# Performance work log

Measured on AMD Instinct MI355X. Metric: run time of the kernel, lower is better.

## Reference

```python
import jax, jax.numpy as jnp
import numpy as np

T, B, K = 512, 512, 8
V, H, NL, NLAB = 5, 30, 4, 3


def setup_inputs() -> dict:
    key = jax.random.key(0)
    ks = jax.random.split(key, 12)
    s = 0.1
    return {
        "x": jax.random.randint(ks[0], (T, B, K), 0, V),
        "weight_of_x": jax.random.uniform(ks[1], (T, B, K), dtype=jnp.float32),
        "embed": jax.random.normal(ks[2], (V, H), dtype=jnp.float32) * s,
        "lstm_Wih": jax.random.normal(ks[3], (NL, 4 * H, H), dtype=jnp.float32) * s,
        "lstm_Whh": jax.random.normal(ks[4], (NL, 4 * H, H), dtype=jnp.float32) * s,
        "lstm_bih": jax.random.normal(ks[5], (NL, 4 * H), dtype=jnp.float32) * s,
        "lstm_bhh": jax.random.normal(ks[6], (NL, 4 * H), dtype=jnp.float32) * s,
        "attn_W1": jax.random.normal(ks[7], (H, 64), dtype=jnp.float32) * s,
        "attn_b1": jnp.zeros((64,), jnp.float32),
        "attn_W2": jax.random.normal(ks[8], (64, 1), dtype=jnp.float32) * s,
        "attn_b2": jnp.zeros((1,), jnp.float32),
        "fc_W": jax.random.normal(ks[9], (H, NLAB), dtype=jnp.float32) * s,
        "fc_b": jnp.zeros((NLAB,), jnp.float32),
    }


def _lstm_layer(xs, Wih, Whh, bih, bhh):
    # xs: (T, B, H_in); PyTorch gate order i, f, g, o
    b = bih + bhh
    Bsz = xs.shape[1]
    h0 = jnp.zeros((Bsz, Whh.shape[1]), xs.dtype)

    def step(carry, xt):
        h, c = carry
        gates = xt @ Wih.T + h @ Whh.T + b  # (B, 4H)
        i, f, g, o = jnp.split(gates, 4, axis=-1)
        i, f, o = jax.nn.sigmoid(i), jax.nn.sigmoid(f), jax.nn.sigmoid(o)
        g = jnp.tanh(g)
        c = f * c + i * g
        h = o * jnp.tanh(c)
        return (h, c), h

    _, hs = jax.lax.scan(step, (h0, h0), xs)
    return hs  # (T, B, H)


def reference(x, weight_of_x, embed, lstm_Wih, lstm_Whh, lstm_bih, lstm_bhh,
              attn_W1, attn_b1, attn_W2, attn_b2, fc_W, fc_b):
    # embedding + weighted mean pooling over K
    e = embed[x] * weight_of_x[..., None]          # (T, B, K, H)
    e = jax.nn.relu(e)
    seq = jnp.mean(e, axis=2)                      # (T, B, H)

    # 4-layer LSTM (loop over fixed num_layers)
    out = seq
    for l in range(lstm_Wih.shape[0]):
        out = _lstm_layer(out, lstm_Wih[l], lstm_Whh[l], lstm_bih[l], lstm_bhh[l])

    # attention pooling over time
    enc = jnp.transpose(out, (1, 0, 2))            # (B, T, H)
    energy = jax.nn.relu(enc @ attn_W1 + attn_b1) @ attn_W2 + attn_b2  # (B, T, 1)
    weights = jax.nn.softmax(energy[..., 0], axis=1)  # (B, T)
    pooled = jnp.sum(enc * weights[..., None], axis=1)  # (B, H)

    # dropout is identity in eval mode
    logit = jax.nn.softmax(pooled @ fc_W + fc_b, axis=1)  # (B, 3)
    return logit
```

## Files before the change

kernel.cpp:

```cpp
#include <hip/hip_runtime.h>

#define TT 512
#define BB 512
#define KK 8
#define HH 30
#define GG 120
#define NLAYER 4

__device__ __forceinline__ float rcp_f(float x) { return __builtin_amdgcn_rcpf(x); }
__device__ __forceinline__ float rdlane_f(float v, int l) {
    return __int_as_float(__builtin_amdgcn_readlane(__float_as_int(v), l));
}
__device__ __forceinline__ float2 pk_fma_v(float2 a, float2 b, float2 c) {
    float2 d;
    asm("v_pk_fma_f32 %0, %1, %2, %3" : "=v"(d) : "v"(a), "v"(b), "v"(c));
    return d;
}
__device__ __forceinline__ float2 pk_fma_s(float2 a, float2 bs, float2 c) {
    float2 d;
    asm("v_pk_fma_f32 %0, %1, %2, %3" : "=v"(d) : "v"(a), "s"(bs), "v"(c));
    return d;
}
__device__ __forceinline__ float2 pk_add(float2 a, float2 b) {
    float2 d;
    asm("v_pk_add_f32 %0, %1, %2" : "=v"(d) : "v"(a), "v"(b));
    return d;
}
__device__ __forceinline__ float swap32_hi(float x) {
    float a = x, b = x;
    asm("v_permlane32_swap_b32 %0, %1" : "+v"(a), "+v"(b));
    return b;
}

__global__ __launch_bounds__(256) __attribute__((amdgpu_waves_per_eu(2, 2)))
void rnn_fused(
    const int*   __restrict__ xin,  const float* __restrict__ wxin,
    const float* __restrict__ embed,
    const float* __restrict__ Wih,  const float* __restrict__ Whh,
    const float* __restrict__ bih,  const float* __restrict__ bhh,
    const float* __restrict__ W1,   const float* __restrict__ b1,
    const float* __restrict__ W2,   const float* __restrict__ b2,
    const float* __restrict__ fcW,  const float* __restrict__ fcb,
    float* __restrict__ out)
{
    __shared__ alignas(16) float hstore[TT * HH];
    __shared__ alignas(16) float seqring[2][16][32];
    __shared__ alignas(16) int   ringx[4][16][KK];
    __shared__ alignas(16) float ringw[4][16][KK];
    __shared__ alignas(16) float hring[NLAYER][8][32];
    __shared__ alignas(16) float re_s[5 * HH];
    __shared__ alignas(16) float energy_s[TT];
    __shared__ float red_s[16];
    __shared__ float part_s[8][HH];
    __shared__ float pooled_s[HH];
    __shared__ float logits_s[3];
    __shared__ int   sync_s[8];

    const int tid  = threadIdx.x;
    const int wv   = tid >> 6;
    const int lane = tid & 63;
    const int b    = blockIdx.x;
    volatile int* vs = sync_s;

    if (tid < 8) sync_s[tid] = 0;
    if (tid < 5 * HH) re_s[tid] = fmaxf(embed[tid], 0.0f);
    {
        float4 z; z.x = 0.f; z.y = 0.f; z.z = 0.f; z.w = 0.f;
        ((float4*)hring)[tid] = z;
    }

    int4 hx = {0,0,0,0}; float4 hw = {0,0,0,0};
    if (wv == 0 && lane < 32) {
        const int r = lane >> 1, hf = lane & 1;
        #pragma unroll
        for (int cc = 0; cc < 2; ++cc) {
            long off = ((long)(16 * cc + r) * BB + b) * KK + hf * 4;
            *(int4*)(&ringx[cc][r][hf * 4])   = *(const int4*)(xin  + off);
            *(float4*)(&ringw[cc][r][hf * 4]) = *(const float4*)(wxin + off);
        }
        long off2 = ((long)(32 + r) * BB + b) * KK + hf * 4;
        hx = *(const int4*)(xin  + off2);
        hw = *(const float4*)(wxin + off2);
    }

    const int half = lane >> 5;
    const int q31  = lane & 31;
    const int qq   = (q31 < HH) ? q31 : (HH - 1);
    const int rA   = qq + half * HH;
    const int rB   = rA + 60;
    float2 wihA[15], wihB[15], whhA[15], whhB[15];
    {
        const float* WihL = Wih + wv * GG * HH;
        const float* WhhL = Whh + wv * GG * HH;
        #pragma unroll
        for (int kk = 0; kk < 15; ++kk) {
            wihA[kk] = *(const float2*)(WihL + rA * HH + 2 * kk);
            wihB[kk] = *(const float2*)(WihL + rB * HH + 2 * kk);
            whhA[kk] = *(const float2*)(WhhL + rA * HH + 2 * kk);
            whhB[kk] = *(const float2*)(WhhL + rB * HH + 2 * kk);
        }
    }
    const float biasA = bih[wv * GG + rA] + bhh[wv * GG + rA];
    const float biasB = bih[wv * GG + rB] + bhh[wv * GG + rB];
    const float mBneg = (lane < 32) ? -2.0f : -1.0f;
    const float aB    = (lane < 32) ?  2.0f :  1.0f;
    const float dB    = (lane < 32) ? -1.0f :  0.0f;

    __syncthreads();

    float c_val = 0.0f;

    auto do_step = [&](int t) {
        const float* xsrc = (wv == 0) ? &seqring[(t >> 4) & 1][t & 15][0]
                                      : &hring[wv - 1][t & 7][0];
        const float* hsrc = &hring[wv][(t + 7) & 7][0];
        float2 ah0 = {0.f,0.f}, ah1 = {0.f,0.f};
        float2 ax0 = {0.f,0.f}, ax1 = {0.f,0.f};
        #pragma unroll
        for (int k = 0; k < 15; ++k) {
            const float2 xp = *(const float2*)(xsrc + 2 * k);
            const float2 hp = *(const float2*)(hsrc + 2 * k);
            ax0 = pk_fma_v(wihA[k], xp, ax0);
            ax1 = pk_fma_v(wihB[k], xp, ax1);
            ah0 = pk_fma_v(whhA[k], hp, ah0);
            ah1 = pk_fma_v(whhB[k], hp, ah1);
        }
        const float2 s0 = pk_add(ax0, ah0);
        const float2 s1 = pk_add(ax1, ah1);
        const float gA = s0.x + s0.y + biasA;
        const float gB = s1.x + s1.y + biasB;
        const float actA = rcp_f(1.0f + __expf(-gA));
        const float sB   = rcp_f(1.0f + __expf(gB * mBneg));
        const float actB = fmaf(aB, sB, dB);
        const float fI = swap32_hi(actA);
        const float oI = swap32_hi(actB);
        c_val = fmaf(fI, c_val, actA * actB);
        const float tC = fmaf(2.0f, rcp_f(1.0f + __expf(-2.0f * c_val)), -1.0f);
        const float hv = oI * tC;
        if (lane < HH) {
            hring[wv][t & 7][lane] = hv;
            if (wv == NLAYER - 1) hstore[t * HH + lane] = hv;
        }
    };

    for (int T0 = 0; T0 < TT; T0 += 4) {
        if (wv == 0) {
            if ((T0 & 15) == 0) {
                const int c = T0 >> 4;
                if (lane < 32) {
                    const int r = lane >> 1, hf = lane & 1;
                    if (c <= 29) {
                        const int sl = (c + 2) & 3;
                        *(int4*)(&ringx[sl][r][hf * 4])   = hx;
                        *(float4*)(&ringw[sl][r][hf * 4]) = hw;
                    }
                    if (c <= 28) {
                        long off = ((long)(16 * (c + 3) + r) * BB + b) * KK + hf * 4;
                        hx = *(const int4*)(xin  + off);
                        hw = *(const float4*)(wxin + off);
                    }
                }
                const int sl = c & 3, par = c & 1;
                #pragma unroll
                for (int rr = 0; rr < 8; ++rr) {
                    const int o = lane + rr * 64;
                    if (o < 480) {
                        const int tr = o / HH, j = o - tr * HH;
                        int4   xa = *(const int4*)(&ringx[sl][tr][0]);
                        int4   xb = *(const int4*)(&ringx[sl][tr][4]);
                        float4 wa = *(const float4*)(&ringw[sl][tr][0]);
                        float4 wb = *(const float4*)(&ringw[sl][tr][4]);
                        float acc = re_s[xa.x * HH + j] * wa.x;
                        acc = fmaf(re_s[xa.y * HH + j], wa.y, acc);
                        acc = fmaf(re_s[xa.z * HH + j], wa.z, acc);
                        acc = fmaf(re_s[xa.w * HH + j], wa.w, acc);
                        acc = fmaf(re_s[xb.x * HH + j], wb.x, acc);
                        acc = fmaf(re_s[xb.y * HH + j], wb.y, acc);
                        acc = fmaf(re_s[xb.z * HH + j], wb.z, acc);
                        acc = fmaf(re_s[xb.w * HH + j], wb.w, acc);
                        seqring[par][tr][j] = acc * 0.125f;
                    }
                }
                __threadfence_block();
            }
        } else {
            while (vs[wv - 1] < T0 + 4) __builtin_amdgcn_s_sleep(2);
        }
        if (wv < NLAYER - 1) {
            while (vs[4 + wv + 1] < T0 - 4) __builtin_amdgcn_s_sleep(2);
        }
        __threadfence_block();
        do_step(T0 + 0);
        do_step(T0 + 1);
        do_step(T0 + 2);
        do_step(T0 + 3);
        __threadfence_block();
        if (lane == 0) {
            if (wv < NLAYER - 1) vs[wv]     = T0 + 4;
            if (wv > 0)          vs[4 + wv] = T0 + 4;
        }
    }

    __syncthreads();

    {
        float w1cx[15], w1cy[15];
        #pragma unroll
        for (int k = 0; k < 15; ++k) {
            w1cx[k] = W1[(2 * k) * 64 + lane];
            w1cy[k] = W1[(2 * k + 1) * 64 + lane];
        }
        const float b1v = b1[lane];
        const float w2v = W2[lane];
        const float b2v = b2[0];
        #pragma unroll
        for (int pass = 0; pass < 2; ++pass) {
            const int t = wv * 128 + pass * 64 + lane;
            float2 h2[15];
            #pragma unroll
            for (int k = 0; k < 15; ++k)
                h2[k] = *(const float2*)(hstore + t * HH + 2 * k);
            float e = b2v;
            for (int u = 0; u < 64; ++u) {
                float2 acc = {0.f, 0.f};
                #pragma unroll
                for (int k = 0; k < 15; ++k) {
                    float2 wp;
                    wp.x = rdlane_f(w1cx[k], u);
                    wp.y = rdlane_f(w1cy[k], u);
                    acc = pk_fma_s(h2[k], wp, acc);
                }
                const float su = acc.x + acc.y + rdlane_f(b1v, u);
                e = fmaf(fmaxf(su, 0.0f), rdlane_f(w2v, u), e);
            }
            energy_s[t] = e;
        }
    }
    __syncthreads();

    float mx = -3.0e38f;
    for (int i = tid; i < TT; i += 256) mx = fmaxf(mx, energy_s[i]);
    #pragma unroll
    for (int m = 1; m < 64; m <<= 1) mx = fmaxf(mx, __shfl_xor(mx, m, 64));
    if (lane == 0) red_s[wv] = mx;
    __syncthreads();
    mx = fmaxf(fmaxf(red_s[0], red_s[1]), fmaxf(red_s[2], red_s[3]));
    float ssum = 0.0f;
    for (int i = tid; i < TT; i += 256) {
        float ev = __expf(energy_s[i] - mx);
        energy_s[i] = ev;
        ssum += ev;
    }
    #pragma unroll
    for (int m = 1; m < 64; m <<= 1) ssum += __shfl_xor(ssum, m, 64);
    if (lane == 0) red_s[8 + wv] = ssum;
    __syncthreads();
    const float invS = rcp_f(red_s[8] + red_s[9] + red_s[10] + red_s[11]);

    {
        const int g = tid >> 5, jj = tid & 31;
        if (jj < HH) {
            float part = 0.0f;
            for (int t = g; t < TT; t += 8)
                part = fmaf(energy_s[t] * invS, hstore[t * HH + jj], part);
            part_s[g][jj] = part;
        }
    }
    __syncthreads();
    if (tid < HH) {
        float pv = 0.0f;
        #pragma unroll
        for (int q = 0; q < 8; ++q) pv += part_s[q][tid];
        pooled_s[tid] = pv;
    }
    __syncthreads();

    if (tid < 3) {
        float acc = fcb[tid];
        #pragma unroll
        for (int k = 0; k < HH; ++k) acc = fmaf(pooled_s[k], fcW[k * 3 + tid], acc);
        logits_s[tid] = acc;
    }
    __syncthreads();
    if (tid == 0) {
        float l0 = logits_s[0], l1 = logits_s[1], l2 = logits_s[2];
        float m3 = fmaxf(l0, fmaxf(l1, l2));
        float e0 = __expf(l0 - m3), e1 = __expf(l1 - m3), e2 = __expf(l2 - m3);
        float inv = rcp_f(e0 + e1 + e2);
        out[b * 3 + 0] = e0 * inv; out[b * 3 + 1] = e1 * inv; out[b * 3 + 2] = e2 * inv;
    }
}

extern "C" void kernel_launch(void* const* d_in, const int* in_sizes, int n_in,
                              void* d_out, int out_size, void* d_ws, size_t ws_size,
                              hipStream_t stream)
{
    (void)in_sizes; (void)n_in; (void)d_ws; (void)ws_size; (void)out_size;
    rnn_fused<<<BB, 256, 0, stream>>>(
        (const int*)  d_in[0],  (const float*)d_in[1],  (const float*)d_in[2],
        (const float*)d_in[3],  (const float*)d_in[4],  (const float*)d_in[5],
        (const float*)d_in[6],  (const float*)d_in[7],  (const float*)d_in[8],
        (const float*)d_in[9],  (const float*)d_in[10], (const float*)d_in[11],
        (const float*)d_in[12], (float*)d_out);
}
```

Before: 496.9 us.

## Process two batch samples per block with barrier-synchronised layer wavefront

Each block now handles two batch elements, so every wave reuses its register-resident LSTM weights across two independent recurrences per step. This gives the dependent chain more instruction-level parallelism and halves the grid to 256 blocks. The spin-wait flag synchronisation between layer waves is replaced by a skewed epoch loop with a block-wide __syncthreads per 4-step group. LDS use roughly doubles (hstore alone becomes about 120KB), and waves_per_eu drops to 1. With only 256 blocks on a GPU with many CUs, a large part of the machine may sit idle, and each block's serial latency roughly doubles.

Result: slower. 695.7 us (+40.0%).

```diff
diff --git a/kernel.cpp b/kernel.cpp
--- a/kernel.cpp
+++ b/kernel.cpp
@@ -6,6 +6,7 @@
 #define HH 30
 #define GG 120
 #define NLAYER 4
+#define SPB 2
 
 __device__ __forceinline__ float rcp_f(float x) { return __builtin_amdgcn_rcpf(x); }
 __device__ __forceinline__ float rdlane_f(float v, int l) {
@@ -32,7 +33,7 @@
     return b;
 }
 
-__global__ __launch_bounds__(256) __attribute__((amdgpu_waves_per_eu(2, 2)))
+__global__ __launch_bounds__(256) __attribute__((amdgpu_waves_per_eu(1, 1)))
 void rnn_fused(
     const int*   __restrict__ xin,  const float* __restrict__ wxin,
     const float* __restrict__ embed,
@@ -43,44 +44,47 @@
     const float* __restrict__ fcW,  const float* __restrict__ fcb,
     float* __restrict__ out)
 {
-    __shared__ alignas(16) float hstore[TT * HH];
-    __shared__ alignas(16) float seqring[2][16][32];
-    __shared__ alignas(16) int   ringx[4][16][KK];
-    __shared__ alignas(16) float ringw[4][16][KK];
-    __shared__ alignas(16) float hring[NLAYER][8][32];
+    __shared__ alignas(16) float hstore[SPB][TT * HH];
+    __shared__ alignas(16) float seqring[SPB][2][16][32];
+    __shared__ alignas(16) int   ringx[SPB][4][16][KK];
+    __shared__ alignas(16) float ringw[SPB][4][16][KK];
+    __shared__ alignas(16) float hring[SPB][NLAYER][8][32];
     __shared__ alignas(16) float re_s[5 * HH];
     __shared__ alignas(16) float energy_s[TT];
     __shared__ float red_s[16];
     __shared__ float part_s[8][HH];
     __shared__ float pooled_s[HH];
     __shared__ float logits_s[3];
-    __shared__ int   sync_s[8];
 
     const int tid  = threadIdx.x;
     const int wv   = tid >> 6;
     const int lane = tid & 63;
-    const int b    = blockIdx.x;
-    volatile int* vs = sync_s;
-
-    if (tid < 8) sync_s[tid] = 0;
+    const int b0   = blockIdx.x * SPB;
+
     if (tid < 5 * HH) re_s[tid] = fmaxf(embed[tid], 0.0f);
     {
         float4 z; z.x = 0.f; z.y = 0.f; z.z = 0.f; z.w = 0.f;
-        ((float4*)hring)[tid] = z;
-    }
-
-    int4 hx = {0,0,0,0}; float4 hw = {0,0,0,0};
+        ((float4*)hring)[tid]       = z;
+        ((float4*)hring)[tid + 256] = z;
+    }
+
+    int4 hx[SPB]; float4 hw[SPB];
+    #pragma unroll
+    for (int s = 0; s < SPB; ++s) { hx[s] = {0,0,0,0}; hw[s] = {0,0,0,0}; }
     if (wv == 0 && lane < 32) {
         const int r = lane >> 1, hf = lane & 1;
         #pragma unroll
-        for (int cc = 0; cc < 2; ++cc) {
-            long off = ((long)(16 * cc + r) * BB + b) * KK + hf * 4;
-            *(int4*)(&ringx[cc][r][hf * 4])   = *(const int4*)(xin  + off);
-            *(float4*)(&ringw[cc][r][hf * 4]) = *(const float4*)(wxin + off);
-        }
-        long off2 = ((long)(32 + r) * BB + b) * KK + hf * 4;
-        hx = *(const int4*)(xin  + off2);
-        hw = *(const float4*)(wxin + off2);
+        for (int s = 0; s < SPB; ++s) {
+            #pragma unroll
+            for (int cc = 0; cc < 2; ++cc) {
+                long off = ((long)(16 * cc + r) * BB + (b0 + s)) * KK + hf * 4;
+                *(int4*)(&ringx[s][cc][r][hf * 4])   = *(const int4*)(xin  + off);
+                *(float4*)(&ringw[s][cc][r][hf * 4]) = *(const float4*)(wxin + off);
+            }
+            long off2 = ((long)(32 + r) * BB + (b0 + s)) * KK + hf * 4;
+            hx[s] = *(const int4*)(xin  + off2);
+            hw[s] = *(const float4*)(wxin + off2);
+        }
     }
 
     const int half = lane >> 5;
@@ -108,118 +112,134 @@
 
     __syncthreads();
 
-    float c_val = 0.0f;
+    float c_val[SPB];
+    #pragma unroll
+    for (int s = 0; s < SPB; ++s) c_val[s] = 0.0f;
 
     auto do_step = [&](int t) {
-        const float* xsrc = (wv == 0) ? &seqring[(t >> 4) & 1][t & 15][0]
-                                      : &hring[wv - 1][t & 7][0];
-        const float* hsrc = &hring[wv][(t + 7) & 7][0];
-        float2 ah0 = {0.f,0.f}, ah1 = {0.f,0.f};
-        float2 ax0 = {0.f,0.f}, ax1 = {0.f,0.f};
+        const float* xsrc[SPB];
+        const float* hsrc[SPB];
+        #pragma unroll
+        for (int s = 0; s < SPB; ++s) {
+            xsrc[s] = (wv == 0) ? &seqring[s][(t >> 4) & 1][t & 15][0]
+                                : &hring[s][wv - 1][t & 7][0];
+            hsrc[s] = &hring[s][wv][(t + 7) & 7][0];
+        }
+        float2 ax0[SPB], ax1[SPB], ah0[SPB], ah1[SPB];
+        #pragma unroll
+        for (int s = 0; s < SPB; ++s) {
+            ax0[s] = {0.f,0.f}; ax1[s] = {0.f,0.f};
+            ah0[s] = {0.f,0.f}; ah1[s] = {0.f,0.f};
+        }
         #pragma unroll
         for (int k = 0; k < 15; ++k) {
-            const float2 xp = *(const float2*)(xsrc + 2 * k);
-            const float2 hp = *(const float2*)(hsrc + 2 * k);
-            ax0 = pk_fma_v(wihA[k], xp, ax0);
-            ax1 = pk_fma_v(wihB[k], xp, ax1);
-            ah0 = pk_fma_v(whhA[k], hp, ah0);
-            ah1 = pk_fma_v(whhB[k], hp, ah1);
-        }
-        const float2 s0 = pk_add(ax0, ah0);
-        const float2 s1 = pk_add(ax1, ah1);
-        const float gA = s0.x + s0.y + biasA;
-        const float gB = s1.x + s1.y + biasB;
-        const float actA = rcp_f(1.0f + __expf(-gA));
-        const float sB   = rcp_f(1.0f + __expf(gB * mBneg));
-        const float actB = fmaf(aB, sB, dB);
-        const float fI = swap32_hi(actA);
-        const float oI = swap32_hi(actB);
-        c_val = fmaf(fI, c_val, actA * actB);
-        const float tC = fmaf(2.0f, rcp_f(1.0f + __expf(-2.0f * c_val)), -1.0f);
-        const float hv = oI * tC;
-        if (lane < HH) {
-            hring[wv][t & 7][lane] = hv;
-            if (wv == NLAYER - 1) hstore[t * HH + lane] = hv;
+            #pragma unroll
+            for (int s = 0; s < SPB; ++s) {
+                const float2 xp = *(const float2*)(xsrc[s] + 2 * k);
+                const float2 hp = *(const float2*)(hsrc[s] + 2 * k);
+                ax0[s] = pk_fma_v(wihA[k], xp, ax0[s]);
+                ax1[s] = pk_fma_v(wihB[k], xp, ax1[s]);
+                ah0[s] = pk_fma_v(whhA[k], hp, ah0[s]);
+                ah1[s] = pk_fma_v(whhB[k], hp, ah1[s]);
+            }
+        }
+        #pragma unroll
+        for (int s = 0; s < SPB; ++s) {
+            const float2 s0 = pk_add(ax0[s], ah0[s]);
+            const float2 s1 = pk_add(ax1[s], ah1[s]);
+            const float gA = s0.x + s0.y + biasA;
+            const float gB = s1.x + s1.y + biasB;
+            const float actA = rcp_f(1.0f + __expf(-gA));
+            const float sB   = rcp_f(1.0f + __expf(gB * mBneg));
+            const float actB = fmaf(aB, sB, dB);
+            const float fI = swap32_hi(actA);
+            const float oI = swap32_hi(actB);
+            c_val[s] = fmaf(fI, c_val[s], actA * actB);
+            const float tC = fmaf(2.0f, rcp_f(1.0f + __expf(-2.0f * c_val[s])), -1.0f);
+            const float hv = oI * tC;
+            if (lane < HH) {
+                hring[s][wv][t & 7][lane] = hv;
+                if (wv == NLAYER - 1) hstore[s][t * HH + lane] = hv;
+            }
         }
     };
 
-    for (int T0 = 0; T0 < TT; T0 += 4) {
-        if (wv == 0) {
-            if ((T0 & 15) == 0) {
+    const int NGROUP = TT / 4;
+    const int NEPOCH = NGROUP + NLAYER - 1;
+    for (int n = 0; n < NEPOCH; ++n) {
+        const int g = n - wv;
+        if (g >= 0 && g < NGROUP) {
+            const int T0 = 4 * g;
+            if (wv == 0 && (T0 & 15) == 0) {
                 const int c = T0 >> 4;
                 if (lane < 32) {
                     const int r = lane >> 1, hf = lane & 1;
-                    if (c <= 29) {
-                        const int sl = (c + 2) & 3;
-                        *(int4*)(&ringx[sl][r][hf * 4])   = hx;
-                        *(float4*)(&ringw[sl][r][hf * 4]) = hw;
-                    }
-                    if (c <= 28) {
-                        long off = ((long)(16 * (c + 3) + r) * BB + b) * KK + hf * 4;
-                        hx = *(const int4*)(xin  + off);
-                        hw = *(const float4*)(wxin + off);
+                    #pragma unroll
+                    for (int s = 0; s < SPB; ++s) {
+                        if (c <= 29) {
+                            const int sl = (c + 2) & 3;
+                            *(int4*)(&ringx[s][sl][r][hf * 4])   = hx[s];
+                            *(float4*)(&ringw[s][sl][r][hf * 4]) = hw[s];
+                        }
+                        if (c <= 28) {
+                            long off = ((long)(16 * (c + 3) + r) * BB + (b0 + s)) * KK + hf * 4;
+                            hx[s] = *(const int4*)(xin  + off);
+                            hw[s] = *(const float4*)(wxin + off);
+                        }
                     }
                 }
                 const int sl = c & 3, par = c & 1;
                 #pragma unroll
-                for (int rr = 0; rr < 8; ++rr) {
-                    const int o = lane + rr * 64;
-                    if (o < 480) {
-                        const int tr = o / HH, j = o - tr * HH;
-                        int4   xa = *(const int4*)(&ringx[sl][tr][0]);
-                        int4   xb = *(const int4*)(&ringx[sl][tr][4]);
-                        float4 wa = *(const float4*)(&ringw[sl][tr][0]);
-                        float4 wb = *(const float4*)(&ringw[sl][tr][4]);
-                        float acc = re_s[xa.x * HH + j] * wa.x;
-                        acc = fmaf(re_s[xa.y * HH + j], wa.y, acc);
-                        acc = fmaf(re_s[xa.z * HH + j], wa.z, acc);
-                        acc = fmaf(re_s[xa.w * HH + j], wa.w, acc);
-                        acc = fmaf(re_s[xb.x * HH + j], wb.x, acc);
-                        acc = fmaf(re_s[xb.y * HH + j], wb.y, acc);
-                        acc = fmaf(re_s[xb.z * HH + j], wb.z, acc);
-                        acc = fmaf(re_s[xb.w * HH + j], wb.w, acc);
-                        seqring[par][tr][j] = acc * 0.125f;
+                for (int s = 0; s < SPB; ++s) {
+                    #pragma unroll
+                    for (int rr = 0; rr < 8; ++rr) {
+                        const int o = lane + rr * 64;
+                        if (o < 480) {
+                            const int tr = o / HH, j = o - tr * HH;
+                            int4   xa = *(const int4*)(&ringx[s][sl][tr][0]);
+                            int4   xb = *(const int4*)(&ringx[s][sl][tr][4]);
+                            float4 wa = *(const float4*)(&ringw[s][sl][tr][0]);
+                            float4 wb = *(const float4*)(&ringw[s][sl][tr][4]);
+                            float acc = re_s[xa.x * HH + j] * wa.x;
+                            acc = fmaf(re_s[xa.y * HH + j], wa.y, acc);
+                            acc = fmaf(re_s[xa.z * HH + j], wa.z, acc);
+                            acc = fmaf(re_s[xa.w * HH + j], wa.w, acc);
+                            acc = fmaf(re_s[xb.x * HH + j], wb.x, acc);
+                            acc = fmaf(re_s[xb.y * HH + j], wb.y, acc);
+                            acc = fmaf(re_s[xb.z * HH + j], wb.z, acc);
+                            acc = fmaf(re_s[xb.w * HH + j], wb.w, acc);
+                            seqring[s][par][tr][j] = acc * 0.125f;
+                        }
                     }
                 }
-                __threadfence_block();
-            }
-        } else {
-            while (vs[wv - 1] < T0 + 4) __builtin_amdgcn_s_sleep(2);
-        }
-        if (wv < NLAYER - 1) {
-            while (vs[4 + wv + 1] < T0 - 4) __builtin_amdgcn_s_sleep(2);
-        }
-        __threadfence_block();
-        do_step(T0 + 0);
-        do_step(T0 + 1);
-        do_step(T0 + 2);
-        do_step(T0 + 3);
-        __threadfence_block();
-        if (lane == 0) {
-            if (wv < NLAYER - 1) vs[wv]     = T0 + 4;
-            if (wv > 0)          vs[4 + wv] = T0 + 4;
-        }
-    }
-
-    __syncthreads();
-
-    {
-        float w1cx[15], w1cy[15];
-        #pragma unroll
-        for (int k = 0; k < 15; ++k) {
-            w1cx[k] = W1[(2 * k) * 64 + lane];
-            w1cy[k] = W1[(2 * k + 1) * 64 + lane];
-        }
-        const float b1v = b1[lane];
-        const float w2v = W2[lane];
-        const float b2v = b2[0];
+            }
+            do_step(T0 + 0);
+            do_step(T0 + 1);
+            do_step(T0 + 2);
+            do_step(T0 + 3);
+        }
+        __syncthreads();
+    }
+
+
+    float w1cx[15], w1cy[15];
+    #pragma unroll
+    for (int k = 0; k < 15; ++k) {
+        w1cx[k] = W1[(2 * k) * 64 + lane];
+        w1cy[k] = W1[(2 * k + 1) * 64 + lane];
+    }
+    const float b1v = b1[lane];
+    const float w2v = W2[lane];
+    const float b2v = b2[0];
+
+    for (int s = 0; s < SPB; ++s) {
         #pragma unroll
         for (int pass = 0; pass < 2; ++pass) {
             const int t = wv * 128 + pass * 64 + lane;
             float2 h2[15];
             #pragma unroll
             for (int k = 0; k < 15; ++k)
-                h2[k] = *(const float2*)(hstore + t * HH + 2 * k);
+                h2[k] = *(const float2*)(&hstore[s][t * HH + 2 * k]);
             float e = b2v;
             for (int u = 0; u < 64; ++u) {
                 float2 acc = {0.f, 0.f};
@@ -235,59 +255,61 @@
             }
             energy_s[t] = e;
         }
-    }
-    __syncthreads();
-
-    float mx = -3.0e38f;
-    for (int i = tid; i < TT; i += 256) mx = fmaxf(mx, energy_s[i]);
-    #pragma unroll
-    for (int m = 1; m < 64; m <<= 1) mx = fmaxf(mx, __shfl_xor(mx, m, 64));
-    if (lane == 0) red_s[wv] = mx;
-    __syncthreads();
-    mx = fmaxf(fmaxf(red_s[0], red_s[1]), fmaxf(red_s[2], red_s[3]));
-    float ssum = 0.0f;
-    for (int i = tid; i < TT; i += 256) {
-        float ev = __expf(energy_s[i] - mx);
-        energy_s[i] = ev;
-        ssum += ev;
-    }
-    #pragma unroll
-    for (int m = 1; m < 64; m <<= 1) ssum += __shfl_xor(ssum, m, 64);
-    if (lane == 0) red_s[8 + wv] = ssum;
-    __syncthreads();
-    const float invS = rcp_f(red_s[8] + red_s[9] + red_s[10] + red_s[11]);
-
-    {
-        const int g = tid >> 5, jj = tid & 31;
-        if (jj < HH) {
-            float part = 0.0f;
-            for (int t = g; t < TT; t += 8)
-                part = fmaf(energy_s[t] * invS, hstore[t * HH + jj], part);
-            part_s[g][jj] = part;
-        }
-    }
-    __syncthreads();
-    if (tid < HH) {
-        float pv = 0.0f;
-        #pragma unroll
-        for (int q = 0; q < 8; ++q) pv += part_s[q][tid];
-        pooled_s[tid] = pv;
-    }
-    __syncthreads();
-
-    if (tid < 3) {
-        float acc = fcb[tid];
-        #pragma unroll
-        for (int k = 0; k < HH; ++k) acc = fmaf(pooled_s[k], fcW[k * 3 + tid], acc);
-        logits_s[tid] = acc;
-    }
-    __syncthreads();
-    if (tid == 0) {
-        float l0 = logits_s[0], l1 = logits_s[1], l2 = logits_s[2];
-        float m3 = fmaxf(l0, fmaxf(l1, l2));
-        float e0 = __expf(l0 - m3), e1 = __expf(l1 - m3), e2 = __expf(l2 - m3);
-        float inv = rcp_f(e0 + e1 + e2);
-        out[b * 3 + 0] = e0 * inv; out[b * 3 + 1] = e1 * inv; out[b * 3 + 2] = e2 * inv;
+        __syncthreads();
+
+        float mx = -3.0e38f;
+        for (int i = tid; i < TT; i += 256) mx = fmaxf(mx, energy_s[i]);
+        #pragma unroll
+        for (int m = 1; m < 64; m <<= 1) mx = fmaxf(mx, __shfl_xor(mx, m, 64));
+        if (lane == 0) red_s[wv] = mx;
+        __syncthreads();
+        mx = fmaxf(fmaxf(red_s[0], red_s[1]), fmaxf(red_s[2], red_s[3]));
+        float ssum = 0.0f;
+        for (int i = tid; i < TT; i += 256) {
+            float ev = __expf(energy_s[i] - mx);
+            energy_s[i] = ev;
+            ssum += ev;
+        }
+        #pragma unroll
+        for (int m = 1; m < 64; m <<= 1) ssum += __shfl_xor(ssum, m, 64);
+        if (lane == 0) red_s[8 + wv] = ssum;
+        __syncthreads();
+        const float invS = rcp_f(red_s[8] + red_s[9] + red_s[10] + red_s[11]);
+
+        {
+            const int g = tid >> 5, jj = tid & 31;
+            if (jj < HH) {
+                float part = 0.0f;
+                for (int t = g; t < TT; t += 8)
+                    part = fmaf(energy_s[t] * invS, hstore[s][t * HH + jj], part);
+                part_s[g][jj] = part;
+            }
+        }
+        __syncthreads();
+        if (tid < HH) {
+            float pv = 0.0f;
+            #pragma unroll
+            for (int q = 0; q < 8; ++q) pv += part_s[q][tid];
+            pooled_s[tid] = pv;
+        }
+        __syncthreads();
+
+        if (tid < 3) {
+            float acc = fcb[tid];
+            #pragma unroll
+            for (int k = 0; k < HH; ++k) acc = fmaf(pooled_s[k], fcW[k * 3 + tid], acc);
+            logits_s[tid] = acc;
+        }
+        __syncthreads();
+        if (tid == 0) {
+            float l0 = logits_s[0], l1 = logits_s[1], l2 = logits_s[2];
+            float m3 = fmaxf(l0, fmaxf(l1, l2));
+            float e0 = __expf(l0 - m3), e1 = __expf(l1 - m3), e2 = __expf(l2 - m3);
+            float inv = rcp_f(e0 + e1 + e2);
+            const int bo = (b0 + s) * 3;
+            out[bo + 0] = e0 * inv; out[bo + 1] = e1 * inv; out[bo + 2] = e2 * inv;
+        }
+        __syncthreads();
     }
 }
 
@@ -296,7 +318,7 @@
                               hipStream_t stream)
 {
     (void)in_sizes; (void)n_in; (void)d_ws; (void)ws_size; (void)out_size;
-    rnn_fused<<<BB, 256, 0, stream>>>(
+    rnn_fused<<<BB / SPB, 256, 0, stream>>>(
         (const int*)  d_in[0],  (const float*)d_in[1],  (const float*)d_in[2],
         (const float*)d_in[3],  (const float*)d_in[4],  (const float*)d_in[5],
         (const float*)d_in[6],  (const float*)d_in[7],  (const float*)d_in[8],
```
